# Kernel optimization log

Measured on AMD Instinct MI355X. Metric: run time of the kernel, lower is better.

## Reference

```python
import jax, jax.numpy as jnp
import numpy as np

N_NODES, N_EDGES, F_IN, HID, PROJ, N_CLS, N_GRAPHS, T_EMB = 50000, 800000, 128, 128, 512, 32, 256, 768
EPS_BN, EPS_LN = 1e-5, 1e-5


def setup_inputs() -> dict:
    key = jax.random.key(0)
    ks = jax.random.split(key, 24)
    s = 0.05
    inp = {
        "x": jax.random.normal(ks[0], (N_NODES, F_IN), jnp.float32),
        "edge_index": jax.random.randint(ks[1], (2, N_EDGES), 0, N_NODES),
        "batch": jnp.sort(jax.random.randint(ks[2], (N_NODES,), 0, N_GRAPHS)),
        "text_feats": jax.random.normal(ks[3], (N_GRAPHS, T_EMB), jnp.float32),
        # 4 stacked GCN layers (all 128->128), each with BatchNorm affine params
        "gcn_W": jax.random.normal(ks[4], (4, F_IN, HID), jnp.float32) * s,
        "gcn_b": jnp.zeros((4, HID), jnp.float32),
        "bn_g": jnp.ones((4, HID), jnp.float32),
        "bn_b": jnp.zeros((4, HID), jnp.float32),
        # graph projection head
        "gpj_W1": jax.random.normal(ks[5], (HID, PROJ), jnp.float32) * s,
        "gpj_b1": jnp.zeros((PROJ,), jnp.float32),
        "gpj_W2": jax.random.normal(ks[6], (PROJ, PROJ), jnp.float32) * s,
        "gpj_b2": jnp.zeros((PROJ,), jnp.float32),
        "gpj_g": jnp.ones((PROJ,), jnp.float32),
        "gpj_be": jnp.zeros((PROJ,), jnp.float32),
        "gcl_W": jax.random.normal(ks[7], (PROJ, N_CLS), jnp.float32) * s,
        "gcl_b": jnp.zeros((N_CLS,), jnp.float32),
        # text projection head
        "tpj_W1": jax.random.normal(ks[8], (T_EMB, PROJ), jnp.float32) * s,
        "tpj_b1": jnp.zeros((PROJ,), jnp.float32),
        "tpj_W2": jax.random.normal(ks[9], (PROJ, PROJ), jnp.float32) * s,
        "tpj_b2": jnp.zeros((PROJ,), jnp.float32),
        "tpj_g": jnp.ones((PROJ,), jnp.float32),
        "tpj_be": jnp.zeros((PROJ,), jnp.float32),
        "tcl_W": jax.random.normal(ks[10], (PROJ, N_CLS), jnp.float32) * s,
        "tcl_b": jnp.zeros((N_CLS,), jnp.float32),
    }
    return inp


def _gcn_layer(x, src, dst, dnorm, W, b):
    # PyG GCNConv with self-loops and symmetric normalization
    xw = x @ W  # [N, H]
    coef = dnorm[src] * dnorm[dst]  # [E]
    agg = jax.ops.segment_sum(xw[src] * coef[:, None], dst, num_segments=N_NODES)
    agg = agg + xw * (dnorm * dnorm)[:, None]  # self-loop contribution
    return agg + b


def _batch_norm(x, g, b):
    mu = jnp.mean(x, axis=0)
    var = jnp.mean((x - mu) ** 2, axis=0)
    return (x - mu) * jax.lax.rsqrt(var + EPS_BN) * g + b


def _projection_head(x, W1, b1, W2, b2, g, be):
    projected = x @ W1 + b1
    h = jax.nn.gelu(projected, approximate=False)
    h = h @ W2 + b2
    h = h + projected  # residual (dropout in eval mode = identity)
    mu = jnp.mean(h, axis=-1, keepdims=True)
    var = jnp.mean((h - mu) ** 2, axis=-1, keepdims=True)
    return (h - mu) * jax.lax.rsqrt(var + EPS_LN) * g + be


def reference(x, edge_index, batch, text_feats, gcn_W, gcn_b, bn_g, bn_b,
              gpj_W1, gpj_b1, gpj_W2, gpj_b2, gpj_g, gpj_be, gcl_W, gcl_b,
              tpj_W1, tpj_b1, tpj_W2, tpj_b2, tpj_g, tpj_be, tcl_W, tcl_b):
    src, dst = edge_index[0], edge_index[1]
    deg = jax.ops.segment_sum(jnp.ones((N_EDGES,), x.dtype), dst, num_segments=N_NODES) + 1.0
    dnorm = jax.lax.rsqrt(deg)
    h = x
    for i in range(4):  # input block, 2 hidden blocks, output block
        h = _gcn_layer(h, src, dst, dnorm, gcn_W[i], gcn_b[i])
        h = jax.nn.leaky_relu(h, negative_slope=0.01)
        h = _batch_norm(h, bn_g[i], bn_b[i])
    # global mean pool over graphs
    sums = jax.ops.segment_sum(h, batch, num_segments=N_GRAPHS)
    cnts = jax.ops.segment_sum(jnp.ones((N_NODES,), h.dtype), batch, num_segments=N_GRAPHS)
    g_emb = sums / jnp.maximum(cnts, 1.0)[:, None]  # [G, HID]

    graph_proj = _projection_head(g_emb, gpj_W1, gpj_b1, gpj_W2, gpj_b2, gpj_g, gpj_be)
    graph_logp = jax.nn.log_softmax(graph_proj @ gcl_W + gcl_b, axis=-1)

    text_proj = _projection_head(text_feats, tpj_W1, tpj_b1, tpj_W2, tpj_b2, tpj_g, tpj_be)
    text_logp = jax.nn.log_softmax(text_proj @ tcl_W + tcl_b, axis=-1)

    return (graph_proj, text_proj, graph_logp, text_logp)
```

## Files before the change

### kernel.cpp

```cpp
#include <hip/hip_runtime.h>
#include <hip/hip_bf16.h>

#define N_NODES 50000
#define N_EDGES 800000
#define F_IN    128
#define HID     128
#define PROJ    512
#define N_CLS   32
#define N_GRAPHS 256
#define T_EMB   768
#define NB_SCAN ((N_NODES + 255) / 256)
#define DBINS   1024
#define NBROW   ((N_NODES + 63) / 64)
#define NBG2    ((NBROW + 1) / 2)
#define SHW     6250
#define ESLICE  ((N_EDGES + 4095) / 4096)

typedef __attribute__((ext_vector_type(8))) short bf16x8;
typedef __attribute__((ext_vector_type(4))) float f32x4;

__device__ __forceinline__ float bf2f(unsigned short u) {
    unsigned v = ((unsigned)u) << 16;
    return __uint_as_float(v);
}
__device__ __forceinline__ unsigned short f2us(float v) {
    __hip_bfloat16 b = __float2bfloat16(v);
    union { __hip_bfloat16 b; unsigned short u; } c; c.b = b; return c.u;
}

__global__ __launch_bounds__(256) void k_deg(const int* __restrict__ ei,
                                             int* __restrict__ cnt, int nE) {
    int bx = blockIdx.x;
    int s = bx & 7;
    int slice = bx >> 3;
    int lo = s * SHW, hi = lo + SHW;
    int base = slice * 4096 + threadIdx.x;
#pragma unroll 4
    for (int u = 0; u < 16; u++) {
        int e = base + u * 256;
        if (e < nE) {
            int d = ei[nE + e];
            if (d >= lo && d < hi) atomicAdd(cnt + d, 1);
        }
    }
}

__global__ __launch_bounds__(256) void k_scan1(const int* __restrict__ cnt,
    int* __restrict__ rowstart, float* __restrict__ dnorm, int* __restrict__ bsum)
{
    __shared__ int ps[256];
    int t = threadIdx.x;
    int i = blockIdx.x * 256 + t;
    int c = (i < N_NODES) ? cnt[i] : 0;
    if (i < N_NODES) dnorm[i] = rsqrtf((float)c + 1.0f);
    ps[t] = c;
    __syncthreads();
    for (int off = 1; off < 256; off <<= 1) {
        int v = (t >= off) ? ps[t - off] : 0;
        __syncthreads();
        ps[t] += v;
        __syncthreads();
    }
    if (i < N_NODES) rowstart[i] = ps[t] - c;
    if (t == 255) bsum[blockIdx.x] = ps[255];
}

__global__ __launch_bounds__(256) void k_scan2(int* __restrict__ bsum) {
    __shared__ int ps[256];
    int t = threadIdx.x;
    int v = (t < NB_SCAN) ? bsum[t] : 0;
    ps[t] = v;
    __syncthreads();
    for (int off = 1; off < 256; off <<= 1) {
        int u = (t >= off) ? ps[t - off] : 0;
        __syncthreads();
        ps[t] += u;
        __syncthreads();
    }
    if (t < NB_SCAN) bsum[t] = ps[t] - v;
}

__global__ __launch_bounds__(256) void k_scan3(int* __restrict__ rowstart,
    const int* __restrict__ bsum, const int* __restrict__ cnt,
    int* __restrict__ dhist)
{
    __shared__ int lh[DBINS];
    int t = threadIdx.x;
    for (int k = t; k < DBINS; k += 256) lh[k] = 0;
    __syncthreads();
    int i = blockIdx.x * 256 + t;
    if (i < N_NODES) {
        rowstart[i] += bsum[blockIdx.x];
        atomicAdd(&lh[min(cnt[i], DBINS - 1)], 1);
    }
    if (i == 0) rowstart[N_NODES] = N_EDGES;
    __syncthreads();
    for (int k = t; k < DBINS; k += 256) {
        int v = lh[k];
        if (v) atomicAdd(dhist + k, v);
    }
}

__global__ __launch_bounds__(256) void k_dscan(const int* __restrict__ dhist,
                                               int* __restrict__ doff) {
    __shared__ int part[256];
    __shared__ int binv[DBINS];
    int t = threadIdx.x;
    int base = t * 4;
    int g0 = dhist[DBINS - 1 - (base + 0)];
    int g1 = dhist[DBINS - 1 - (base + 1)];
    int g2 = dhist[DBINS - 1 - (base + 2)];
    int g3 = dhist[DBINS - 1 - (base + 3)];
    int s = g0 + g1 + g2 + g3;
    part[t] = s;
    __syncthreads();
    for (int off = 1; off < 256; off <<= 1) {
        int v = (t >= off) ? part[t - off] : 0;
        __syncthreads();
        part[t] += v;
        __syncthreads();
    }
    int run = part[t] - s;
    binv[base + 0] = run; run += g0;
    binv[base + 1] = run; run += g1;
    binv[base + 2] = run; run += g2;
    binv[base + 3] = run; run += g3;
    __syncthreads();
    for (int k = t; k < DBINS; k += 256) doff[DBINS - 1 - k] = binv[k];
}

__global__ __launch_bounds__(1024) void k_dperm(const int* __restrict__ cnt,
    int* __restrict__ doff, int* __restrict__ rowperm)
{
    __shared__ int lh[DBINS];
    __shared__ int lbase[DBINS];
    int t = threadIdx.x;
    if (t < DBINS) lh[t] = 0;
    __syncthreads();
    int i = blockIdx.x * 1024 + t;
    int bin = 0, lrank = 0;
    bool ok = i < N_NODES;
    if (ok) {
        bin = min(cnt[i], DBINS - 1);
        lrank = atomicAdd(&lh[bin], 1);
    }
    __syncthreads();
    if (t < DBINS) {
        int v = lh[t];
        if (v) lbase[t] = atomicAdd(doff + t, v);
    }
    __syncthreads();
    if (ok) rowperm[lbase[bin] + lrank] = i;
}

__global__ __launch_bounds__(256) void k_fill(const int* __restrict__ ei,
    const int* __restrict__ rowstart, int* __restrict__ cursor,
    int* __restrict__ srcl, int nE)
{
    int bx = blockIdx.x;
    int s = bx & 7;
    int slice = bx >> 3;
    int lo = s * SHW, hi = lo + SHW;
    int base = slice * 4096 + threadIdx.x;
#pragma unroll 4
    for (int u = 0; u < 16; u++) {
        int e = base + u * 256;
        if (e < nE) {
            int d = ei[nE + e];
            if (d >= lo && d < hi) {
                int pos = rowstart[d] + atomicAdd(cursor + d, 1);
                srcl[pos] = ei[e];
            }
        }
    }
}

__global__ void k_prep(const float* __restrict__ W, unsigned short* __restrict__ Wt,
                       const int* __restrict__ batch, int* __restrict__ gstart) {
    int t = blockIdx.x * 256 + threadIdx.x;
    if (t < 4 * 128 * 128) {
        int l = t >> 14;
        int k = (t >> 7) & 127;
        int n = t & 127;
        Wt[(size_t)l * 16384 + n * 128 + k] = f2us(W[(size_t)l * 16384 + k * 128 + n]);
    } else {
        int r = t - 4 * 128 * 128;
        if (r <= N_NODES) {
            int b  = (r < N_NODES) ? batch[r] : N_GRAPHS;
            int bp = (r > 0) ? batch[r - 1] : -1;
            for (int g = bp + 1; g <= b && g <= N_GRAPHS; g++) gstart[g] = r;
        }
    }
}

__global__ __launch_bounds__(256) void k_gcn_mm_mfma(const void* __restrict__ inp,
    const unsigned short* __restrict__ Wt,
    const float* __restrict__ stats, const float* __restrict__ bng,
    const float* __restrict__ bnb, const float* __restrict__ dnorm,
    unsigned short* __restrict__ ph, int n)
{
    __shared__ __align__(16) unsigned short Bs[128][136];
    __shared__ float scs[128], shs[128];
    int t = threadIdx.x;
    int row0 = blockIdx.x * 64;

    if (stats && t < 128) {
        float inv_n = 1.0f / (float)N_NODES;
        float mu = stats[t] * inv_n;
        float var = stats[128 + t] * inv_n - mu * mu;
        float rs = rsqrtf(var + 1e-5f);
        float sc = rs * bng[t];
        scs[t] = sc;
        shs[t] = bnb[t] - mu * sc;
    }
#pragma unroll
    for (int i = 0; i < 8; i++) {
        int c = t + i * 256;
        int nn = c >> 4;
        int k8 = (c & 15) * 8;
        *(uint4*)&Bs[nn][k8] = *(const uint4*)(Wt + (size_t)nn * 128 + k8);
    }
    __syncthreads();

    int w = t >> 6, lane = t & 63;
    int m = lane & 15, quad = lane >> 4;
    int arow = row0 + w * 16 + m;
    bool rowok = arow < n;

    bf16x8 afrag[4];
    if (!stats) {
        const float* inf = (const float*)inp;
#pragma unroll
        for (int ki = 0; ki < 4; ki++) {
            int k8 = ki * 32 + quad * 8;
            float4 v0 = make_float4(0.f, 0.f, 0.f, 0.f);
            float4 v1 = make_float4(0.f, 0.f, 0.f, 0.f);
            if (rowok) {
                v0 = *(const float4*)(inf + (size_t)arow * 128 + k8);
                v1 = *(const float4*)(inf + (size_t)arow * 128 + k8 + 4);
            }
            union { unsigned short u[8]; bf16x8 v; } pk;
            pk.u[0] = f2us(v0.x); pk.u[1] = f2us(v0.y); pk.u[2] = f2us(v0.z); pk.u[3] = f2us(v0.w);
            pk.u[4] = f2us(v1.x); pk.u[5] = f2us(v1.y); pk.u[6] = f2us(v1.z); pk.u[7] = f2us(v1.w);
            afrag[ki] = pk.v;
        }
    } else {
        const unsigned short* inb = (const unsigned short*)inp;
#pragma unroll
        for (int ki = 0; ki < 4; ki++) {
            int k8 = ki * 32 + quad * 8;
            uint4 raw = make_uint4(0, 0, 0, 0);
            if (rowok) raw = *(const uint4*)(inb + (size_t)arow * 128 + k8);
            unsigned rr[4] = { raw.x, raw.y, raw.z, raw.w };
            union { unsigned short u[8]; bf16x8 v; } pk;
#pragma unroll
            for (int j = 0; j < 4; j++) {
                int f0 = k8 + 2 * j, f1 = k8 + 2 * j + 1;
                float a0 = bf2f((unsigned short)rr[j]) * scs[f0] + shs[f0];
                float a1 = bf2f((unsigned short)(rr[j] >> 16)) * scs[f1] + shs[f1];
                pk.u[2 * j] = f2us(a0);
                pk.u[2 * j + 1] = f2us(a1);
            }
            afrag[ki] = pk.v;
        }
    }

    f32x4 acc[8];
#pragma unroll
    for (int nt = 0; nt < 8; nt++) acc[nt] = (f32x4){0.f, 0.f, 0.f, 0.f};
#pragma unroll
    for (int ki = 0; ki < 4; ki++) {
#pragma unroll
        for (int nt = 0; nt < 8; nt++) {
            bf16x8 b = *(const bf16x8*)&Bs[nt * 16 + m][ki * 32 + quad * 8];
            acc[nt] = __builtin_amdgcn_mfma_f32_16x16x32_bf16(afrag[ki], b, acc[nt], 0, 0, 0);
        }
    }

    float dn[4];
#pragma unroll
    for (int reg = 0; reg < 4; reg++) {
        int gr = row0 + w * 16 + quad * 4 + reg;
        dn[reg] = (gr < n) ? dnorm[gr] : 0.f;
    }

    __syncthreads();
#pragma unroll
    for (int nt = 0; nt < 8; nt++) {
#pragma unroll
        for (int reg = 0; reg < 4; reg++) {
            Bs[w * 16 + quad * 4 + reg][nt * 16 + m] = f2us(acc[nt][reg] * dn[reg]);
        }
    }
    __syncthreads();
#pragma unroll
    for (int i = 0; i < 4; i++) {
        int idx = t + i * 256;
        int r = idx >> 4;
        int c8 = (idx & 15) * 8;
        int gr = row0 + r;
        int ch = c8 >> 5;
        int off = c8 & 31;
        if (gr < n)
            *(uint4*)(ph + (size_t)ch * (N_NODES * 32) + (size_t)gr * 32 + off)
                = *(const uint4*)&Bs[r][c8];
    }
}

__global__ __launch_bounds__(256) void k_gather_c(const uint4* __restrict__ ph128,
    const int* __restrict__ srcl, const int* __restrict__ rowstart,
    const int* __restrict__ rowperm, const float* __restrict__ dnorm,
    const float* __restrict__ bias, unsigned short* __restrict__ outbb,
    float* __restrict__ stats, int n)
{
    const int EMAX = N_EDGES - 1;
    __shared__ float bsm[32], bqm[32];
    int t = threadIdx.x;
    if (t < 32) { bsm[t] = 0.f; bqm[t] = 0.f; }
    __syncthreads();

    int bx = blockIdx.x;
    int xcd = bx & 7;
    int c = xcd >> 1;
    int rb = (bx >> 3) * 2 + (xcd & 1);
    if (rb >= NBROW) return;
    int lane = t & 63;
    int w = t >> 6;
    int grp = lane >> 2;
    int l4 = lane & 3;
    int idx = rb * 64 + w * 16 + grp;
    bool rok = idx < n;
    int r = rok ? rowperm[idx] : 0;
    int start = rowstart[r];
    int deg = rowstart[r + 1] - start;
    float dnr = dnorm[r];
    if (!rok) { deg = 0; dnr = 0.f; }
    int len = deg + 1;

    const uint4* phc = ph128 + (size_t)c * (N_NODES * 4);

    float bi[8];
#pragma unroll
    for (int k = 0; k < 8; k++) bi[k] = bias[c * 32 + l4 * 8 + k];

    float a[8];
#pragma unroll
    for (int k = 0; k < 8; k++) a[k] = 0.f;

    for (int j = 0; j < len; j += 4) {
        uint4 uv[4];
#pragma unroll
        for (int u = 0; u < 4; u++) {
            int i = j + u;
            int sl = srcl[min(start + i, EMAX)];
            int s = (i < deg) ? sl : r;
            uv[u] = phc[(size_t)s * 4 + l4];
        }
#pragma unroll
        for (int u = 0; u < 4; u++) {
            int i = j + u;
            float wt = (i < len) ? 1.f : 0.f;
            unsigned rr[4] = { uv[u].x, uv[u].y, uv[u].z, uv[u].w };
#pragma unroll
            for (int d = 0; d < 4; d++) {
                a[2 * d]     += wt * bf2f((unsigned short)rr[d]);
                a[2 * d + 1] += wt * bf2f((unsigned short)(rr[d] >> 16));
            }
        }
    }

    float v[8];
#pragma unroll
    for (int k = 0; k < 8; k++) {
        float x = a[k] * dnr + bi[k];
        v[k] = x > 0.f ? x : 0.01f * x;
    }
    if (rok) {
        union { unsigned short us[8]; uint4 u; } ov;
#pragma unroll
        for (int k = 0; k < 8; k++) ov.us[k] = f2us(v[k]);
        *(uint4*)(outbb + (size_t)r * 128 + c * 32 + l4 * 8) = ov.u;
    } else {
#pragma unroll
        for (int k = 0; k < 8; k++) v[k] = 0.f;
    }

    float q[8];
#pragma unroll
    for (int k = 0; k < 8; k++) q[k] = v[k] * v[k];
#pragma unroll
    for (int mk = 4; mk < 64; mk <<= 1) {
#pragma unroll
        for (int k = 0; k < 8; k++) {
            v[k] += __shfl_xor(v[k], mk, 64);
            q[k] += __shfl_xor(q[k], mk, 64);
        }
    }
    if (grp == 0) {
#pragma unroll
        for (int k = 0; k < 8; k++) {
            atomicAdd(&bsm[l4 * 8 + k], v[k]);
            atomicAdd(&bqm[l4 * 8 + k], q[k]);
        }
    }
    __syncthreads();
    if (t < 32) {
        atomicAdd(&stats[c * 32 + t], bsm[t]);
        atomicAdd(&stats[128 + c * 32 + t], bqm[t]);
    }
}

__global__ __launch_bounds__(256) void k_pool2(const unsigned short* __restrict__ outbb,
    const int* __restrict__ gstart, const float* __restrict__ stats,
    const float* __restrict__ bng, const float* __restrict__ bnb,
    float* __restrict__ gemb)
{
    __shared__ float scs[128], shs[128];
    int g = blockIdx.x;
    int t = threadIdx.x;
    if (t < 128) {
        float inv_n = 1.0f / (float)N_NODES;
        float mu = stats[t] * inv_n;
        float var = stats[128 + t] * inv_n - mu * mu;
        float rs = rsqrtf(var + 1e-5f);
        float sc = rs * bng[t];
        scs[t] = sc;
        shs[t] = bnb[t] - mu * sc;
    }
    __syncthreads();
    int f = t & 127;
    int half = t >> 7;
    int start = gstart[g], end = gstart[g + 1];
    int cnt = end - start;
    float s0 = 0.f, s1 = 0.f, s2 = 0.f, s3 = 0.f;
    int r = start + half;
    for (; r + 6 < end; r += 8) {
        s0 += bf2f(outbb[(size_t)(r    ) * 128 + f]);
        s1 += bf2f(outbb[(size_t)(r + 2) * 128 + f]);
        s2 += bf2f(outbb[(size_t)(r + 4) * 128 + f]);
        s3 += bf2f(outbb[(size_t)(r + 6) * 128 + f]);
    }
    for (; r < end; r += 2) s0 += bf2f(outbb[(size_t)r * 128 + f]);
    float sum = (s0 + s1) + (s2 + s3);
    __shared__ float sb[256];
    sb[t] = sum;
    __syncthreads();
    if (t < 128) {
        float tot = sb[t] + sb[t + 128];
        float v = (cnt > 0) ? (tot / (float)cnt) * scs[f] + shs[f] : 0.f;
        gemb[(size_t)g * 128 + f] = v;
    }
}

__global__ __launch_bounds__(256) void k_head1x(const float* __restrict__ gemb,
    const float* __restrict__ textf,
    const float* __restrict__ gW1, const float* __restrict__ tW1,
    float* __restrict__ projg, float* __restrict__ projt6)
{
    __shared__ float ins[8][128];
    int bx = blockIdx.x;
    int kc = blockIdx.z;
    int isT = bx >= 32;
    if (!isT && kc > 0) return;
    int rb = isT ? bx - 32 : bx;
    const float* in = isT ? textf : gemb;
    int K = isT ? T_EMB : HID;
    const float* W = isT ? tW1 : gW1;
    float* outp = isT ? (projt6 + (size_t)kc * (N_GRAPHS * PROJ)) : projg;
    int k0 = kc * 128;

    int t = threadIdx.x;
    {
        int r = t >> 5, k = (t & 31) * 4;
        *(float4*)&ins[r][k] = *(const float4*)(in + (size_t)(rb * 8 + r) * K + k0 + k);
    }
    __syncthreads();
    int col = blockIdx.y * 128 + (t & 127);
    int rg = t >> 7;
    float acc[4] = { 0.f, 0.f, 0.f, 0.f };
    const float* Wp = W + (size_t)k0 * 512 + col;
#pragma unroll 8
    for (int k = 0; k < 128; k++) {
        float w = Wp[(size_t)k * 512];
#pragma unroll
        for (int i = 0; i < 4; i++) acc[i] += ins[rg * 4 + i][k] * w;
    }
#pragma unroll
    for (int i = 0; i < 4; i++) {
        int row = rb * 8 + rg * 4 + i;
        outp[(size_t)row * 512 + col] = acc[i];
    }
}

__global__ __launch_bounds__(256) void k_hprep(const float* __restrict__ projg,
    const float* __restrict__ projt6, const float* __restrict__ gb1,
    const float* __restrict__ tb1, float* __restrict__ prow_buf,
    float* __restrict__ grow_buf)
{
    int idx = (blockIdx.x * 256 + threadIdx.x) * 4;
    int row = idx >> 9;
    int c = idx & 511;
    int isT = row >= N_GRAPHS;
    int lrow = row & (N_GRAPHS - 1);
    const float* b1 = isT ? tb1 : gb1;
    float4 p;
    if (isT) {
        const float* pp = projt6 + (size_t)lrow * 512 + c;
        p = *(const float4*)pp;
#pragma unroll
        for (int s = 1; s < 6; s++) {
            float4 q = *(const float4*)(pp + (size_t)s * (N_GRAPHS * PROJ));
            p.x += q.x; p.y += q.y; p.z += q.z; p.w += q.w;
        }
    } else {
        p = *(const float4*)(projg + (size_t)lrow * 512 + c);
    }
    float4 b = *(const float4*)(b1 + c);
    p.x += b.x; p.y += b.y; p.z += b.z; p.w += b.w;
    *(float4*)(prow_buf + (size_t)row * 512 + c) = p;
    float4 g;
    g.x = 0.5f * p.x * (1.0f + erff(p.x * 0.70710678118f));
    g.y = 0.5f * p.y * (1.0f + erff(p.y * 0.70710678118f));
    g.z = 0.5f * p.z * (1.0f + erff(p.z * 0.70710678118f));
    g.w = 0.5f * p.w * (1.0f + erff(p.w * 0.70710678118f));
    *(float4*)(grow_buf + (size_t)row * 512 + c) = g;
}

__global__ __launch_bounds__(256) void k_head2a(const float* __restrict__ grow_buf,
    const float* __restrict__ gW2, const float* __restrict__ tW2,
    float* __restrict__ h2p)
{
    __shared__ float gs[8][128];
    int rb = blockIdx.x;
    int cc = blockIdx.y;
    int kc = blockIdx.z;
    int isT = rb >= 32;
    const float* W2 = isT ? tW2 : gW2;
    int t = threadIdx.x;
    {
        int r = t >> 5, k4 = (t & 31) * 4;
        *(float4*)&gs[r][k4] =
            *(const float4*)(grow_buf + (size_t)(rb * 8 + r) * 512 + kc * 128 + k4);
    }
    __syncthreads();
    int col = cc * 128 + (t & 127);
    int rg = t >> 7;
    float acc[4] = { 0.f, 0.f, 0.f, 0.f };
    const float* Wp = W2 + (size_t)(kc * 128) * 512 + col;
#pragma unroll 8
    for (int k = 0; k < 128; k++) {
        float w = Wp[(size_t)k * 512];
#pragma unroll
        for (int i = 0; i < 4; i++) acc[i] += gs[rg * 4 + i][k] * w;
    }
#pragma unroll
    for (int i = 0; i < 4; i++) {
        int row = rb * 8 + rg * 4 + i;
        h2p[(size_t)kc * (512 * 512) + (size_t)row * 512 + col] = acc[i];
    }
}

__global__ __launch_bounds__(256) void k_head2b(const float* __restrict__ h2p,
    const float* __restrict__ prow_buf,
    const float* __restrict__ gb2, const float* __restrict__ gg,
    const float* __restrict__ gbe, const float* __restrict__ gclW,
    const float* __restrict__ gclb,
    const float* __restrict__ tb2, const float* __restrict__ tg,
    const float* __restrict__ tbe, const float* __restrict__ tclW,
    const float* __restrict__ tclb,
    float* __restrict__ o_gproj, float* __restrict__ o_tproj,
    float* __restrict__ o_glogp, float* __restrict__ o_tlogp)
{
    __shared__ float onorm[512], red[256];
    __shared__ float part[8][32];
    __shared__ float logits[32];
    __shared__ float mred, lred;
    int bx = blockIdx.x;
    int isT = bx >= N_GRAPHS;
    int row = bx & (N_GRAPHS - 1);
    const float* b2 = isT ? tb2 : gb2;
    const float* g  = isT ? tg  : gg;
    const float* be = isT ? tbe : gbe;
    const float* Wc = isT ? tclW : gclW;
    const float* bc = isT ? tclb : gclb;
    float* oproj = isT ? o_tproj : o_gproj;
    float* ologp = isT ? o_tlogp : o_glogp;

    int t = threadIdx.x;
    int c0 = t, c1 = t + 256;
    size_t base = (size_t)bx * 512;
    float h0 = prow_buf[base + c0] + b2[c0];
    float h1 = prow_buf[base + c1] + b2[c1];
#pragma unroll
    for (int kc = 0; kc < 4; kc++) {
        h0 += h2p[(size_t)kc * (512 * 512) + base + c0];
        h1 += h2p[(size_t)kc * (512 * 512) + base + c1];
    }
    red[t] = h0 + h1;
    __syncthreads();
    for (int s = 128; s > 0; s >>= 1) { if (t < s) red[t] += red[t + s]; __syncthreads(); }
    float mu = red[0] * (1.0f / 512.0f);
    __syncthreads();
    float d0 = h0 - mu, d1 = h1 - mu;
    red[t] = d0 * d0 + d1 * d1;
    __syncthreads();
    for (int s = 128; s > 0; s >>= 1) { if (t < s) red[t] += red[t + s]; __syncthreads(); }
    float rs = rsqrtf(red[0] * (1.0f / 512.0f) + 1e-5f);
    float o0 = d0 * rs * g[c0] + be[c0];
    float o1 = d1 * rs * g[c1] + be[c1];
    onorm[c0] = o0;
    onorm[c1] = o1;
    oproj[(size_t)row * 512 + c0] = o0;
    oproj[(size_t)row * 512 + c1] = o1;
    __syncthreads();

    int c = t & 31, seg = t >> 5;
    float p = 0.f;
    for (int k = seg * 64; k < seg * 64 + 64; k++)
        p += onorm[k] * Wc[(size_t)k * 32 + c];
    part[seg][c] = p;
    __syncthreads();
    if (t < 32) {
        float l = bc[t];
#pragma unroll
        for (int s = 0; s < 8; s++) l += part[s][t];
        logits[t] = l;
    }
    __syncthreads();
    if (t == 0) {
        float m = logits[0];
        for (int i = 1; i < 32; i++) m = fmaxf(m, logits[i]);
        float sum = 0.f;
        for (int i = 0; i < 32; i++) sum += expf(logits[i] - m);
        mred = m; lred = logf(sum);
    }
    __syncthreads();
    if (t < 32) ologp[(size_t)row * 32 + t] = logits[t] - mred - lred;
}

extern "C" void kernel_launch(void* const* d_in, const int* in_sizes, int n_in,
                              void* d_out, int out_size, void* d_ws, size_t ws_size,
                              hipStream_t stream) {
    const float* x     = (const float*)d_in[0];
    const int*   ei    = (const int*)d_in[1];
    const int*   batch = (const int*)d_in[2];
    const float* textf = (const float*)d_in[3];
    const float* gcnW  = (const float*)d_in[4];
    const float* gcnb  = (const float*)d_in[5];
    const float* bng   = (const float*)d_in[6];
    const float* bnb   = (const float*)d_in[7];
    const float* gW1   = (const float*)d_in[8];
    const float* gb1   = (const float*)d_in[9];
    const float* gW2   = (const float*)d_in[10];
    const float* gb2   = (const float*)d_in[11];
    const float* gg    = (const float*)d_in[12];
    const float* gbe   = (const float*)d_in[13];
    const float* gclW  = (const float*)d_in[14];
    const float* gclb  = (const float*)d_in[15];
    const float* tW1   = (const float*)d_in[16];
    const float* tb1   = (const float*)d_in[17];
    const float* tW2   = (const float*)d_in[18];
    const float* tb2   = (const float*)d_in[19];
    const float* tg    = (const float*)d_in[20];
    const float* tbe   = (const float*)d_in[21];
    const float* tclW  = (const float*)d_in[22];
    const float* tclb  = (const float*)d_in[23];

    const int N = N_NODES, E = N_EDGES;
    const int NF = N * HID;

    float* p = (float*)d_ws;
    unsigned short* outbb = (unsigned short*)p; p += NF / 2;
    unsigned short* ph    = (unsigned short*)p; p += NF / 2;
    unsigned short* Wt    = (unsigned short*)p; p += 4 * 16384 / 2;
    float* dnorm    = p; p += N;
    float* gemb     = p; p += N_GRAPHS * HID;
    float* projg    = p; p += N_GRAPHS * PROJ;
    float* projt6   = p; p += 6 * N_GRAPHS * PROJ;
    float* prow_buf = p; p += 512 * PROJ;
    float* grow_buf = p; p += 512 * PROJ;
    float* h2p      = p; p += 4 * 512 * PROJ;
    int* cnt      = (int*)p; p += N;
    int* cursor   = (int*)p; p += N;
    float* stats4 = p; p += 4 * 256;
    int* dhist    = (int*)p; p += DBINS;
    int* rowstart = (int*)p; p += N + 1;
    int* gstart   = (int*)p; p += N_GRAPHS + 1;
    int* bsum     = (int*)p; p += 256;
    int* srcl     = (int*)p; p += E;
    int* doff     = (int*)p; p += DBINS;
    int* rowperm  = (int*)p; p += N;

    float* outp = (float*)d_out;
    float* o_gproj = outp;
    float* o_tproj = outp + N_GRAPHS * PROJ;
    float* o_glogp = o_tproj + N_GRAPHS * PROJ;
    float* o_tlogp = o_glogp + N_GRAPHS * N_CLS;

    hipMemsetAsync(cnt, 0, (size_t)(2 * N + 4 * 256 + DBINS) * sizeof(int), stream);
    k_deg<<<ESLICE * 8, 256, 0, stream>>>(ei, cnt, E);
    k_scan1<<<NB_SCAN, 256, 0, stream>>>(cnt, rowstart, dnorm, bsum);
    k_scan2<<<1, 256, 0, stream>>>(bsum);
    k_scan3<<<NB_SCAN, 256, 0, stream>>>(rowstart, bsum, cnt, dhist);
    k_fill<<<ESLICE * 8, 256, 0, stream>>>(ei, rowstart, cursor, srcl, E);
    k_dscan<<<1, 256, 0, stream>>>(dhist, doff);
    k_dperm<<<(N + 1023) / 1024, 1024, 0, stream>>>(cnt, doff, rowperm);
    k_prep<<<(4 * 16384 + N + 1 + 255) / 256, 256, 0, stream>>>(gcnW, Wt, batch, gstart);

    for (int l = 0; l < 4; l++) {
        const void* in = (l == 0) ? (const void*)x : (const void*)outbb;
        const float* st = (l == 0) ? nullptr : stats4 + (l - 1) * 256;
        const float* bg = (l == 0) ? nullptr : bng + (size_t)(l - 1) * HID;
        const float* bb = (l == 0) ? nullptr : bnb + (size_t)(l - 1) * HID;
        k_gcn_mm_mfma<<<(N + 63) / 64, 256, 0, stream>>>(in, Wt + (size_t)l * 16384,
                                                         st, bg, bb, dnorm, ph, N);
        k_gather_c<<<NBG2 * 8, 256, 0, stream>>>((const uint4*)ph, srcl,
                                                 rowstart, rowperm, dnorm,
                                                 gcnb + (size_t)l * HID, outbb,
                                                 stats4 + l * 256, N);
    }

    k_pool2<<<N_GRAPHS, 256, 0, stream>>>(outbb, gstart, stats4 + 3 * 256,
                                          bng + 3 * HID, bnb + 3 * HID, gemb);

    k_head1x<<<dim3(64, 4, 6), 256, 0, stream>>>(gemb, textf, gW1, tW1, projg, projt6);
    k_hprep<<<256, 256, 0, stream>>>(projg, projt6, gb1, tb1, prow_buf, grow_buf);
    k_head2a<<<dim3(64, 4, 4), 256, 0, stream>>>(grow_buf, gW2, tW2, h2p);
    k_head2b<<<512, 256, 0, stream>>>(h2p, prow_buf,
                                      gb2, gg, gbe, gclW, gclb,
                                      tb2, tg, tbe, tclW, tclb,
                                      o_gproj, o_tproj, o_glogp, o_tlogp);
}
```

Baseline: 457.7 us.

## Bin edges by destination shard, pack 16-bit indices and per-row metadata

Replaces the sliced degree and fill passes, which each rescanned all edges per shard, with a single binning pass. That pass writes packed (dst,src) 16-bit pairs into per-shard buffers, and later degree and fill kernels read only their shard. Source lists are stored as 16-bit indices, and per-row start, degree, node id and dnorm are packed into one int4, so the gather does one load per row instead of several dependent ones. The gather loop is also unrolled to 8 edges to issue more independent loads. This relies on node ids fitting in 16 bits and on shard sizes staying under a fixed capacity.

```diff
diff --git a/kernel.cpp b/kernel.cpp
--- a/kernel.cpp
+++ b/kernel.cpp
@@ -14,7 +14,8 @@
 #define NBROW   ((N_NODES + 63) / 64)
 #define NBG2    ((NBROW + 1) / 2)
 #define SHW     6250
-#define ESLICE  ((N_EDGES + 4095) / 4096)
+#define ECAP    131072
+#define NBF     98
 
 typedef __attribute__((ext_vector_type(8))) short bf16x8;
 typedef __attribute__((ext_vector_type(4))) float f32x4;
@@ -28,21 +29,48 @@
     union { __hip_bfloat16 b; unsigned short u; } c; c.b = b; return c.u;
 }
 
-__global__ __launch_bounds__(256) void k_deg(const int* __restrict__ ei,
-                                             int* __restrict__ cnt, int nE) {
-    int bx = blockIdx.x;
-    int s = bx & 7;
-    int slice = bx >> 3;
-    int lo = s * SHW, hi = lo + SHW;
-    int base = slice * 4096 + threadIdx.x;
-#pragma unroll 4
-    for (int u = 0; u < 16; u++) {
+__global__ __launch_bounds__(256) void k_bin(const int* __restrict__ ei,
+    unsigned* __restrict__ ebuf, int* __restrict__ ecur, int nE)
+{
+    __shared__ int lcnt[8], lbase[8], lcur[8];
+    int t = threadIdx.x;
+    if (t < 8) { lcnt[t] = 0; lcur[t] = 0; }
+    __syncthreads();
+    int base = blockIdx.x * 1024 + t;
+    int dd[4], ss[4], sh[4];
+    bool ok[4];
+#pragma unroll
+    for (int u = 0; u < 4; u++) {
         int e = base + u * 256;
-        if (e < nE) {
-            int d = ei[nE + e];
-            if (d >= lo && d < hi) atomicAdd(cnt + d, 1);
-        }
-    }
+        ok[u] = e < nE;
+        int d = ok[u] ? ei[nE + e] : 0;
+        int s = ok[u] ? ei[e] : 0;
+        dd[u] = d; ss[u] = s;
+        sh[u] = d / SHW;
+        if (ok[u]) atomicAdd(&lcnt[sh[u]], 1);
+    }
+    __syncthreads();
+    if (t < 8) lbase[t] = atomicAdd(ecur + t, lcnt[t]);
+    __syncthreads();
+#pragma unroll
+    for (int u = 0; u < 4; u++) {
+        if (ok[u]) {
+            int rank = atomicAdd(&lcur[sh[u]], 1);
+            ebuf[(size_t)sh[u] * ECAP + lbase[sh[u]] + rank] =
+                ((unsigned)dd[u] << 16) | (unsigned)ss[u];
+        }
+    }
+}
+
+__global__ __launch_bounds__(256) void k_degb(const unsigned* __restrict__ ebuf,
+    const int* __restrict__ ecur, int* __restrict__ cnt)
+{
+    int s = blockIdx.x & 7;
+    int bs = blockIdx.x >> 3;
+    int ecnt = ecur[s];
+    const unsigned* eb = ebuf + (size_t)s * ECAP;
+    for (int i = bs * 256 + threadIdx.x; i < ecnt; i += NBF * 256)
+        atomicAdd(cnt + (eb[i] >> 16), 1);
 }
 
 __global__ __launch_bounds__(256) void k_scan1(const int* __restrict__ cnt,
@@ -98,6 +126,22 @@
     for (int k = t; k < DBINS; k += 256) {
         int v = lh[k];
         if (v) atomicAdd(dhist + k, v);
+    }
+}
+
+__global__ __launch_bounds__(256) void k_fillb(const unsigned* __restrict__ ebuf,
+    const int* __restrict__ ecur, const int* __restrict__ rowstart,
+    int* __restrict__ cursor, unsigned short* __restrict__ srcl16)
+{
+    int s = blockIdx.x & 7;
+    int bs = blockIdx.x >> 3;
+    int ecnt = ecur[s];
+    const unsigned* eb = ebuf + (size_t)s * ECAP;
+    for (int i = bs * 256 + threadIdx.x; i < ecnt; i += NBF * 256) {
+        unsigned pk = eb[i];
+        int d = pk >> 16;
+        int pos = rowstart[d] + atomicAdd(cursor + d, 1);
+        srcl16[pos] = (unsigned short)(pk & 0xffffu);
     }
 }
 
@@ -130,7 +174,8 @@
 }
 
 __global__ __launch_bounds__(1024) void k_dperm(const int* __restrict__ cnt,
-    int* __restrict__ doff, int* __restrict__ rowperm)
+    int* __restrict__ doff, const int* __restrict__ rowstart,
+    const float* __restrict__ dnorm, int4* __restrict__ meta)
 {
     __shared__ int lh[DBINS];
     __shared__ int lbase[DBINS];
@@ -138,10 +183,11 @@
     if (t < DBINS) lh[t] = 0;
     __syncthreads();
     int i = blockIdx.x * 1024 + t;
-    int bin = 0, lrank = 0;
+    int bin = 0, lrank = 0, c = 0;
     bool ok = i < N_NODES;
     if (ok) {
-        bin = min(cnt[i], DBINS - 1);
+        c = cnt[i];
+        bin = min(c, DBINS - 1);
         lrank = atomicAdd(&lh[bin], 1);
     }
     __syncthreads();
@@ -150,28 +196,14 @@
         if (v) lbase[t] = atomicAdd(doff + t, v);
     }
     __syncthreads();
-    if (ok) rowperm[lbase[bin] + lrank] = i;
-}
-
-__global__ __launch_bounds__(256) void k_fill(const int* __restrict__ ei,
-    const int* __restrict__ rowstart, int* __restrict__ cursor,
-    int* __restrict__ srcl, int nE)
-{
-    int bx = blockIdx.x;
-    int s = bx & 7;
-    int slice = bx >> 3;
-    int lo = s * SHW, hi = lo + SHW;
-    int base = slice * 4096 + threadIdx.x;
-#pragma unroll 4
-    for (int u = 0; u < 16; u++) {
-        int e = base + u * 256;
-        if (e < nE) {
-            int d = ei[nE + e];
-            if (d >= lo && d < hi) {
-                int pos = rowstart[d] + atomicAdd(cursor + d, 1);
-                srcl[pos] = ei[e];
-            }
-        }
+    if (ok) {
+        int pos = lbase[bin] + lrank;
+        int4 mv;
+        mv.x = i;
+        mv.y = rowstart[i];
+        mv.z = c;
+        mv.w = __float_as_int(dnorm[i]);
+        meta[pos] = mv;
     }
 }
 
@@ -308,8 +340,7 @@
 }
 
 __global__ __launch_bounds__(256) void k_gather_c(const uint4* __restrict__ ph128,
-    const int* __restrict__ srcl, const int* __restrict__ rowstart,
-    const int* __restrict__ rowperm, const float* __restrict__ dnorm,
+    const unsigned short* __restrict__ srcl16, const int4* __restrict__ meta,
     const float* __restrict__ bias, unsigned short* __restrict__ outbb,
     float* __restrict__ stats, int n)
 {
@@ -323,18 +354,15 @@
     int xcd = bx & 7;
     int c = xcd >> 1;
     int rb = (bx >> 3) * 2 + (xcd & 1);
-    if (rb >= NBROW) return;
     int lane = t & 63;
     int w = t >> 6;
     int grp = lane >> 2;
     int l4 = lane & 3;
     int idx = rb * 64 + w * 16 + grp;
     bool rok = idx < n;
-    int r = rok ? rowperm[idx] : 0;
-    int start = rowstart[r];
-    int deg = rowstart[r + 1] - start;
-    float dnr = dnorm[r];
-    if (!rok) { deg = 0; dnr = 0.f; }
+    int4 mv = rok ? meta[idx] : make_int4(0, 0, 0, 0);
+    int r = mv.x, start = mv.y, deg = mv.z;
+    float dnr = rok ? __int_as_float(mv.w) : 0.f;
     int len = deg + 1;
 
     const uint4* phc = ph128 + (size_t)c * (N_NODES * 4);
@@ -347,17 +375,20 @@
 #pragma unroll
     for (int k = 0; k < 8; k++) a[k] = 0.f;
 
-    for (int j = 0; j < len; j += 4) {
-        uint4 uv[4];
-#pragma unroll
-        for (int u = 0; u < 4; u++) {
+    for (int j = 0; j < len; j += 8) {
+        int sl[8];
+#pragma unroll
+        for (int u = 0; u < 8; u++)
+            sl[u] = srcl16[min(start + j + u, EMAX)];
+        uint4 uv[8];
+#pragma unroll
+        for (int u = 0; u < 8; u++) {
             int i = j + u;
-            int sl = srcl[min(start + i, EMAX)];
-            int s = (i < deg) ? sl : r;
+            int s = (i < deg) ? sl[u] : r;
             uv[u] = phc[(size_t)s * 4 + l4];
         }
 #pragma unroll
-        for (int u = 0; u < 4; u++) {
+        for (int u = 0; u < 8; u++) {
             int i = j + u;
             float wt = (i < len) ? 1.f : 0.f;
             unsigned rr[4] = { uv[u].x, uv[u].y, uv[u].z, uv[u].w };
@@ -684,12 +715,14 @@
     int* cursor   = (int*)p; p += N;
     float* stats4 = p; p += 4 * 256;
     int* dhist    = (int*)p; p += DBINS;
+    int* ecur     = (int*)p; p += 8;
     int* rowstart = (int*)p; p += N + 1;
     int* gstart   = (int*)p; p += N_GRAPHS + 1;
     int* bsum     = (int*)p; p += 256;
-    int* srcl     = (int*)p; p += E;
+    unsigned short* srcl16 = (unsigned short*)p; p += E / 2;
+    unsigned* ebuf = (unsigned*)p; p += 8 * ECAP;
     int* doff     = (int*)p; p += DBINS;
-    int* rowperm  = (int*)p; p += N;
+    int4* meta    = (int4*)p; p += 4 * N;
 
     float* outp = (float*)d_out;
     float* o_gproj = outp;
@@ -697,14 +730,15 @@
     float* o_glogp = o_tproj + N_GRAPHS * PROJ;
     float* o_tlogp = o_glogp + N_GRAPHS * N_CLS;
 
-    hipMemsetAsync(cnt, 0, (size_t)(2 * N + 4 * 256 + DBINS) * sizeof(int), stream);
-    k_deg<<<ESLICE * 8, 256, 0, stream>>>(ei, cnt, E);
+    hipMemsetAsync(cnt, 0, (size_t)(2 * N + 4 * 256 + DBINS + 8) * sizeof(int), stream);
+    k_bin<<<(E + 1023) / 1024, 256, 0, stream>>>(ei, ebuf, ecur, E);
+    k_degb<<<NBF * 8, 256, 0, stream>>>(ebuf, ecur, cnt);
     k_scan1<<<NB_SCAN, 256, 0, stream>>>(cnt, rowstart, dnorm, bsum);
     k_scan2<<<1, 256, 0, stream>>>(bsum);
     k_scan3<<<NB_SCAN, 256, 0, stream>>>(rowstart, bsum, cnt, dhist);
-    k_fill<<<ESLICE * 8, 256, 0, stream>>>(ei, rowstart, cursor, srcl, E);
+    k_fillb<<<NBF * 8, 256, 0, stream>>>(ebuf, ecur, rowstart, cursor, srcl16);
     k_dscan<<<1, 256, 0, stream>>>(dhist, doff);
-    k_dperm<<<(N + 1023) / 1024, 1024, 0, stream>>>(cnt, doff, rowperm);
+    k_dperm<<<(N + 1023) / 1024, 1024, 0, stream>>>(cnt, doff, rowstart, dnorm, meta);
     k_prep<<<(4 * 16384 + N + 1 + 255) / 256, 256, 0, stream>>>(gcnW, Wt, batch, gstart);
 
     for (int l = 0; l < 4; l++) {
@@ -714,8 +748,7 @@
         const float* bb = (l == 0) ? nullptr : bnb + (size_t)(l - 1) * HID;
         k_gcn_mm_mfma<<<(N + 63) / 64, 256, 0, stream>>>(in, Wt + (size_t)l * 16384,
                                                          st, bg, bb, dnorm, ph, N);
-        k_gather_c<<<NBG2 * 8, 256, 0, stream>>>((const uint4*)ph, srcl,
-                                                 rowstart, rowperm, dnorm,
+        k_gather_c<<<NBG2 * 8, 256, 0, stream>>>((const uint4*)ph, srcl16, meta,
                                                  gcnb + (size_t)l * HID, outbb,
                                                  stats4 + l * 256, N);
     }
```

Result: faster. 447.0 us (-2.4%).
